# Optimization experiments

Hardware: AMD Instinct MI355X
Metric: run time of the kernel (lower is better)

## Reference

```python
import jax, jax.numpy as jnp
import numpy as np

BN_EPS = 1e-5
STRIDE = 12          # ACCENT_DOWNSAMPLE_STRIDE
NQ = 8               # ACCENT_VQ_QUANTIZERS
K = 256              # ACCENT_VQ_CODEBOOK_SIZE
VQ_D = 16            # ACCENT_VQ_DIM
EMB = 128            # ACCENT_EMBEDDING_DIM


def conv1d(x, w, b, stride=1, padding=0):
    # x: (B, Cin, T), w: (Cout, Cin, Kw)
    y = jax.lax.conv_general_dilated(
        x, w, window_strides=(stride,), padding=[(padding, padding)],
        dimension_numbers=("NCW", "OIW", "NCW"))
    return y + b[None, :, None]


def batchnorm(x, gamma, beta, mean, var):
    # eval-mode BatchNorm1d over channel dim
    inv = jax.lax.rsqrt(var + BN_EPS)
    return (x - mean[None, :, None]) * (inv * gamma)[None, :, None] + beta[None, :, None]


def setup_inputs() -> dict:
    key = jax.random.key(0)
    ks = jax.random.split(key, 12)
    C = 256
    d = {
        "mel_spectrogram": jax.random.normal(ks[0], (16, 80, 4096), jnp.float32),
        "w1": jax.random.normal(ks[1], (C, 80, 5), jnp.float32) * 0.05,
        "b1": jnp.zeros((C,), jnp.float32),
        "g1": jnp.ones((C,), jnp.float32),
        "be1": jnp.zeros((C,), jnp.float32),
        "m1": jax.random.normal(ks[2], (C,), jnp.float32) * 0.1,
        "v1": jax.random.uniform(ks[3], (C,), jnp.float32, 0.5, 1.5),
        "w2": jax.random.normal(ks[4], (C, C, 5), jnp.float32) * 0.03,
        "b2": jnp.zeros((C,), jnp.float32),
        "g2": jnp.ones((C,), jnp.float32),
        "be2": jnp.zeros((C,), jnp.float32),
        "m2": jax.random.normal(ks[5], (C,), jnp.float32) * 0.1,
        "v2": jax.random.uniform(ks[6], (C,), jnp.float32, 0.5, 1.5),
        "wd": jax.random.normal(ks[7], (EMB, C, 2 * STRIDE), jnp.float32) * 0.02,
        "bd": jnp.zeros((EMB,), jnp.float32),
        "wp": jax.random.normal(ks[8], (VQ_D, EMB, 1), jnp.float32) * 0.1,
        "bp": jnp.zeros((VQ_D,), jnp.float32),
        "codebooks": jax.random.normal(ks[9], (NQ, K, VQ_D), jnp.float32) * 0.3,
    }
    return d


def reference(mel_spectrogram, w1, b1, g1, be1, m1, v1,
              w2, b2, g2, be2, m2, v2, wd, bd, wp, bp, codebooks):
    # CNN stack
    x = jax.nn.relu(batchnorm(conv1d(mel_spectrogram, w1, b1, 1, 2), g1, be1, m1, v1))
    x = jax.nn.relu(batchnorm(conv1d(x, w2, b2, 1, 2), g2, be2, m2, v2))
    # Downsample conv: kernel=24, stride=12, pad=6
    e_a_unq = conv1d(x, wd, bd, STRIDE, STRIDE // 2)          # (B, 128, T')
    z = conv1d(e_a_unq, wp, bp, 1, 0)                          # (B, 16, T')
    # RVQ: 8 sequential cdist-argmin-subtract steps
    r = jnp.transpose(z, (0, 2, 1))                            # (B, T', 16)
    idx_list = []
    for q in range(NQ):
        cb = codebooks[q]                                      # (K, 16)
        # squared euclidean distances (B, T', K)
        d = (jnp.sum(r * r, -1, keepdims=True)
             - 2.0 * jnp.einsum("btd,kd->btk", r, cb)
             + jnp.sum(cb * cb, -1))
        idx = jnp.argmin(d, axis=-1)                           # (B, T')
        idx_list.append(idx)
        r = r - cb[idx]                                        # residual update
    indices = jnp.stack(idx_list, axis=0)                      # (NQ, B, T')
    return e_a_unq, indices
```

## Files before the change

kernel.cpp:

```cpp
#include <hip/hip_runtime.h>
#include <math.h>

#define B_    16
#define T_    4096
#define C_    256
#define CIN1  80
#define EMB   128
#define TP    341
#define NPOS  (B_*TP)
#define NQ_   8
#define KCB   256
#define BN_EPS 1e-5

__global__ __launch_bounds__(256) void prep_v7(
    const float* __restrict__ w2, const float* __restrict__ wd,
    const float* __restrict__ b1, const float* __restrict__ g1,
    const float* __restrict__ be1, const float* __restrict__ m1,
    const float* __restrict__ v1,
    const float* __restrict__ b2, const float* __restrict__ g2,
    const float* __restrict__ be2, const float* __restrict__ m2,
    const float* __restrict__ v2,
    float* __restrict__ w2t, float* __restrict__ wdt,
    double* __restrict__ a1, double* __restrict__ bt1,
    double* __restrict__ a2, double* __restrict__ bt2)
{
    int j = blockIdx.x * 256 + threadIdx.x;
    if (j < 256*24*128) wdt[j] = wd[(size_t)(j & 127) * 6144 + (j >> 7)];
    if (j < 256*5*256)  w2t[j] = w2[(size_t)(j & 255) * 1280 + (j >> 8)];
    if (j < 256) {
        double inv1 = 1.0 / sqrt((double)v1[j] + BN_EPS);
        double s1 = (double)g1[j] * inv1;
        a1[j]  = s1;
        bt1[j] = ((double)b1[j] - (double)m1[j]) * s1 + (double)be1[j];
        double inv2 = 1.0 / sqrt((double)v2[j] + BN_EPS);
        double s2 = (double)g2[j] * inv2;
        a2[j]  = s2;
        bt2[j] = ((double)b2[j] - (double)m2[j]) * s2 + (double)be2[j];
    }
}

__device__ __forceinline__ int swz_pair(int col) {
    int bw = col >> 1;
    return ((bw ^ ((bw >> 3) & 7)) << 1);
}
__device__ __forceinline__ int swz_scalar(int col) {
    int bw = col >> 1;
    return (((bw ^ ((bw >> 3) & 7)) << 1) | (col & 1));
}

template<int CIN, typename Tin, bool TR>
__global__ __launch_bounds__(256) void conv5_bn_relu_f64(
    const Tin* __restrict__ in,
    const float* __restrict__ wt,
    const double* __restrict__ alpha, const double* __restrict__ beta,
    double* __restrict__ out)
{
    const int b   = blockIdx.z;
    const int co0 = blockIdx.y * 64;
    const int t0  = blockIdx.x * 128;
    const int tid = threadIdx.x;
    const int tcol = tid & 15;
    const int trow = tid >> 4;

    __shared__ double xs[8][136];
    __shared__ double wsh[40][64];

    double acc[4][8];
    #pragma unroll
    for (int i = 0; i < 4; ++i)
        #pragma unroll
        for (int j = 0; j < 8; ++j) acc[i][j] = 0.0;

    for (int c0 = 0; c0 < CIN; c0 += 8) {
        for (int i = tid; i < 8 * 132; i += 256) {
            int ci = i / 132, col = i % 132;
            int t = t0 - 2 + col;
            double v = 0.0;
            if (t >= 0 && t < T_) v = (double)in[((size_t)(b * CIN + c0 + ci)) * T_ + t];
            xs[ci][swz_scalar(col)] = v;
        }
        for (int i = tid; i < 40 * 64; i += 256) {
            int r = i >> 6, co = i & 63;
            float wv;
            if (TR) wv = wt[(size_t)(c0 * 5 + r) * 256 + co0 + co];
            else    wv = wt[(size_t)(co0 + co) * (CIN * 5) + c0 * 5 + r];
            wsh[r][co] = (double)wv;
        }
        __syncthreads();

        #pragma unroll
        for (int ci = 0; ci < 8; ++ci) {
            double xv[12];
            #pragma unroll
            for (int m = 0; m < 6; ++m) {
                double2 v = *(const double2*)&xs[ci][swz_pair(tcol * 8 + 2 * m)];
                xv[2 * m] = v.x; xv[2 * m + 1] = v.y;
            }
            #pragma unroll
            for (int k = 0; k < 5; ++k) {
                double w0 = wsh[ci * 5 + k][trow * 4 + 0];
                double w1v = wsh[ci * 5 + k][trow * 4 + 1];
                double w2v = wsh[ci * 5 + k][trow * 4 + 2];
                double w3v = wsh[ci * 5 + k][trow * 4 + 3];
                #pragma unroll
                for (int j = 0; j < 8; ++j) {
                    double xq = xv[j + k];
                    acc[0][j] = fma(w0, xq, acc[0][j]);
                    acc[1][j] = fma(w1v, xq, acc[1][j]);
                    acc[2][j] = fma(w2v, xq, acc[2][j]);
                    acc[3][j] = fma(w3v, xq, acc[3][j]);
                }
            }
        }
        __syncthreads();
    }

    const int cobase = co0 + trow * 4;
    const int tg = t0 + tcol * 8;
    #pragma unroll
    for (int i = 0; i < 4; ++i) {
        double a = alpha[cobase + i], bt = beta[cobase + i];
        size_t base = ((size_t)(b * C_ + cobase + i)) * T_ + tg;
        #pragma unroll
        for (int j = 0; j < 8; ++j) {
            double y = fma(acc[i][j], a, bt);
            out[base + j] = y > 0.0 ? y : 0.0;
        }
    }
}

__global__ __launch_bounds__(256) void convd_f64_v6(
    const double* __restrict__ x2,
    const float* __restrict__ wdt,
    double* __restrict__ parts,
    int nb, int nsplit, int cis)
{
    const int bz  = blockIdx.z;
    const int s   = bz % nsplit;
    const int b   = bz / nsplit;
    const int tp0 = blockIdx.x * 64;
    const int tid = threadIdx.x;
    const int tcol = tid & 15;
    const int crow = tid >> 4;

    __shared__ double xs2[2][24][66];
    __shared__ double wsh[48][128];

    double acc[8][4];
    #pragma unroll
    for (int i = 0; i < 8; ++i)
        #pragma unroll
        for (int j = 0; j < 4; ++j) acc[i][j] = 0.0;

    const int tbase = tp0 * 12 - 6;
    const int ci_begin = s * cis;

    for (int c0 = ci_begin; c0 < ci_begin + cis; c0 += 2) {
        for (int i = tid; i < 2 * 780; i += 256) {
            int ci = (i >= 780) ? 1 : 0;
            int c = i - ci * 780;
            int t = tbase + c;
            double v = (t >= 0 && t < T_)
                ? x2[((size_t)(b * 256 + c0 + ci)) * T_ + t] : 0.0;
            int tp = (c * 43691) >> 19;
            int kp = c - tp * 12;
            xs2[ci][kp][tp] = v;
            if (tp >= 1) xs2[ci][kp + 12][tp - 1] = v;
        }
        for (int i = tid; i < 48 * 128; i += 256) {
            int r = i >> 7, c = i & 127;
            wsh[r][c] = (double)wdt[(size_t)(c0 * 24 + r) * 128 + c];
        }
        __syncthreads();

        const double* xb = &xs2[0][0][0] + tcol;
        const double* wb = &wsh[0][0] + crow * 8;
        #pragma unroll
        for (int ci = 0; ci < 2; ++ci) {
            #pragma unroll
            for (int k = 0; k < 24; ++k) {
                double wv[8], xv[4];
                #pragma unroll
                for (int i = 0; i < 8; ++i) wv[i] = wb[(ci * 24 + k) * 128 + i];
                #pragma unroll
                for (int j = 0; j < 4; ++j) xv[j] = xb[(ci * 24 + k) * 66 + 16 * j];
                #pragma unroll
                for (int i = 0; i < 8; ++i)
                    #pragma unroll
                    for (int j = 0; j < 4; ++j)
                        acc[i][j] = fma(wv[i], xv[j], acc[i][j]);
            }
        }
        __syncthreads();
    }

    #pragma unroll
    for (int i = 0; i < 8; ++i) {
        int co = crow * 8 + i;
        #pragma unroll
        for (int j = 0; j < 4; ++j) {
            int tp = tp0 + tcol + 16 * j;
            if (tp < TP)
                parts[(((size_t)s * nb + b) * EMB + co) * TP + tp] = acc[i][j];
        }
    }
}

__global__ __launch_bounds__(256) void convd_combine(
    double* __restrict__ parts,
    const float* __restrict__ bd,
    float* __restrict__ e_out,
    int nb, int b_off, int nsplit)
{
    int idx = blockIdx.x * 256 + threadIdx.x;
    int total = nb * EMB * TP;
    if (idx >= total) return;
    int rem = idx % (EMB * TP);
    int co = rem / TP;
    int b_local = idx / (EMB * TP);
    size_t stride = (size_t)nb * EMB * TP;
    double y = 0.0;
    for (int s = 0; s < nsplit; ++s)
        y += parts[(size_t)s * stride + idx];
    y += (double)bd[co];
    parts[idx] = y;
    e_out[(size_t)b_off * EMB * TP + idx] = (float)y;
}

__global__ __launch_bounds__(128) void zproj_f64(
    const double* __restrict__ ed,
    const float* __restrict__ wp,
    const float* __restrict__ bp,
    double* __restrict__ z)
{
    const int b = blockIdx.y;
    const int t = blockIdx.x * 128 + threadIdx.x;
    __shared__ double wps[16][128];
    for (int i = threadIdx.x; i < 16 * 128; i += 128)
        wps[i >> 7][i & 127] = (double)wp[i];
    __syncthreads();
    if (t >= TP) return;
    double acc[16];
    #pragma unroll
    for (int v = 0; v < 16; ++v) acc[v] = (double)bp[v];
    for (int co = 0; co < 128; ++co) {
        double x = ed[((size_t)(b * EMB + co)) * TP + t];
        #pragma unroll
        for (int v = 0; v < 16; ++v) acc[v] = fma(x, wps[v][co], acc[v]);
    }
    #pragma unroll
    for (int v = 0; v < 16; ++v)
        z[((size_t)(b * TP + t)) * 16 + v] = acc[v];
}

__global__ __launch_bounds__(256) void rvq_f64_v2(
    const double* __restrict__ z,
    const float* __restrict__ cb,
    float* __restrict__ out_idx)
{
    const int pos = blockIdx.x;
    const int tid = threadIdx.x;
    const int lane = tid & 63;
    const int wv = tid >> 6;

    __shared__ double r[16];
    __shared__ double wd_s[4];
    __shared__ int wi_s[4];
    __shared__ int best_s;

    if (tid < 16) r[tid] = z[(size_t)pos * 16 + tid];
    __syncthreads();

    for (int q = 0; q < NQ_; ++q) {
        const float* c = cb + ((size_t)(q * KCB) + tid) * 16;
        double d = 0.0;
        #pragma unroll
        for (int i = 0; i < 16; ++i) {
            double diff = r[i] - (double)c[i];
            d = fma(diff, diff, d);
        }
        int idx = tid;
        #pragma unroll
        for (int sft = 32; sft > 0; sft >>= 1) {
            double d2 = __shfl_down(d, sft, 64);
            int i2 = __shfl_down(idx, sft, 64);
            if (d2 < d || (d2 == d && i2 < idx)) { d = d2; idx = i2; }
        }
        if (lane == 0) { wd_s[wv] = d; wi_s[wv] = idx; }
        __syncthreads();
        if (tid == 0) {
            double bd_ = wd_s[0]; int bi = wi_s[0];
            #pragma unroll
            for (int w = 1; w < 4; ++w) {
                if (wd_s[w] < bd_ || (wd_s[w] == bd_ && wi_s[w] < bi)) {
                    bd_ = wd_s[w]; bi = wi_s[w];
                }
            }
            best_s = bi;
            out_idx[(size_t)q * NPOS + pos] = (float)bi;
        }
        __syncthreads();
        int best = best_s;
        if (tid < 16)
            r[tid] = r[tid] - (double)cb[((size_t)(q * KCB) + best) * 16 + tid];
        __syncthreads();
    }
}

extern "C" void kernel_launch(void* const* d_in, const int* in_sizes, int n_in,
                              void* d_out, int out_size, void* d_ws, size_t ws_size,
                              hipStream_t stream) {
    const float* mel = (const float*)d_in[0];
    const float* w1  = (const float*)d_in[1];
    const float* b1  = (const float*)d_in[2];
    const float* g1  = (const float*)d_in[3];
    const float* be1 = (const float*)d_in[4];
    const float* m1  = (const float*)d_in[5];
    const float* v1  = (const float*)d_in[6];
    const float* w2  = (const float*)d_in[7];
    const float* b2  = (const float*)d_in[8];
    const float* g2  = (const float*)d_in[9];
    const float* be2 = (const float*)d_in[10];
    const float* m2  = (const float*)d_in[11];
    const float* v2  = (const float*)d_in[12];
    const float* wd  = (const float*)d_in[13];
    const float* bd  = (const float*)d_in[14];
    const float* wp  = (const float*)d_in[15];
    const float* bp  = (const float*)d_in[16];
    const float* cb  = (const float*)d_in[17];

    const int nb = 8;
    const int ngrp = B_ / nb;
    const int nsplit = 16;
    const int cis = 256 / nsplit;

    auto al = [](size_t x) { return (x + 255) & ~(size_t)255; };
    const size_t x1_big   = (size_t)nb * C_ * T_ * 8;
    const size_t x1_small = (size_t)4  * C_ * T_ * 8;
    const size_t parts_b  = (size_t)nsplit * nb * EMB * TP * 8;
    const size_t x2_bytes = (size_t)nb * C_ * T_ * 8;
    const size_t tail = al((size_t)256*5*256*4)
                      + al((size_t)256*24*128*4)
                      + 4 * al(2048)
                      + al((size_t)B_ * TP * 16 * 8);
    const size_t need_big = al(x1_big) + al(x2_bytes) + tail;

    const bool big = (ws_size >= need_big);
    const int cc = big ? 8 : 4;
    const size_t shared_bytes = big ? x1_big
                                    : (x1_small > parts_b ? x1_small : parts_b);

    char* ws = (char*)d_ws;
    size_t off = 0;
    auto alloc = [&](size_t bytes) -> char* {
        char* p = ws + off;
        off = (off + bytes + 255) & ~(size_t)255;
        return p;
    };
    char* shared = alloc(shared_bytes);
    double* x1d  = (double*)shared;
    double* parts= (double*)shared;
    double* x2d  = (double*)alloc(x2_bytes);
    float*  w2t  = (float*)alloc((size_t)256*5*256*4);
    float*  wdt  = (float*)alloc((size_t)256*24*128*4);
    double* a1d  = (double*)alloc(2048);
    double* bt1d = (double*)alloc(2048);
    double* a2d  = (double*)alloc(2048);
    double* bt2d = (double*)alloc(2048);
    double* zd   = (double*)alloc((size_t)B_ * TP * 16 * 8);

    float* e_out   = (float*)d_out;
    float* idx_out = (float*)d_out + (size_t)B_ * EMB * TP;

    prep_v7<<<3072, 256, 0, stream>>>(w2, wd, b1, g1, be1, m1, v1,
                                      b2, g2, be2, m2, v2,
                                      w2t, wdt, a1d, bt1d, a2d, bt2d);

    const int comb_blocks = (nb * EMB * TP + 255) / 256;
    for (int g = 0; g < ngrp; ++g) {
        for (int ch = 0; ch < nb / cc; ++ch) {
            int b_abs = g * nb + ch * cc;
            conv5_bn_relu_f64<CIN1, float, false>
                <<<dim3(32, 4, cc), 256, 0, stream>>>(
                mel + (size_t)b_abs * CIN1 * T_, w1, a1d, bt1d,
                x1d + (big ? (size_t)ch * cc * C_ * T_ : 0));
            conv5_bn_relu_f64<C_, double, true>
                <<<dim3(32, 4, cc), 256, 0, stream>>>(
                x1d + (big ? (size_t)ch * cc * C_ * T_ : 0), w2t, a2d, bt2d,
                x2d + (size_t)ch * cc * C_ * T_);
        }
        convd_f64_v6<<<dim3(6, 1, nb * nsplit), 256, 0, stream>>>(
            x2d, wdt, parts, nb, nsplit, cis);
        convd_combine<<<comb_blocks, 256, 0, stream>>>(
            parts, bd, e_out, nb, g * nb, nsplit);
        zproj_f64<<<dim3(3, nb), 128, 0, stream>>>(
            parts, wp, bp, zd + (size_t)g * nb * TP * 16);
    }
    rvq_f64_v2<<<NPOS, 256, 0, stream>>>(zd, cb, idx_out);
}
```

Baseline: 1.902 ms.

## Enlarge register tiles in fp64 conv and downsample kernels for more reuse

The conv5 kernels now compute 256 time steps per block with 4x16 accumulators per thread, and weights are loaded into registers with vectorised double2 reads. The downsample conv processes 128 output positions per block, one input channel per iteration, with 8x8 accumulators per thread and swizzled shared memory. The aim is to raise the FMA-to-shared-load ratio in these fp64 loops and halve the block count. In exchange, register pressure goes up, the launch bounds now request two blocks per SM, and there are fewer blocks to fill the GPU.

Result: faster. 1.781 ms (-6.4%).

```diff
diff --git a/kernel.cpp b/kernel.cpp
--- a/kernel.cpp
+++ b/kernel.cpp
@@ -49,7 +49,7 @@
 }
 
 template<int CIN, typename Tin, bool TR>
-__global__ __launch_bounds__(256) void conv5_bn_relu_f64(
+__global__ __launch_bounds__(256, 2) void conv5_v8(
     const Tin* __restrict__ in,
     const float* __restrict__ wt,
     const double* __restrict__ alpha, const double* __restrict__ beta,
@@ -57,23 +57,23 @@
 {
     const int b   = blockIdx.z;
     const int co0 = blockIdx.y * 64;
-    const int t0  = blockIdx.x * 128;
+    const int t0  = blockIdx.x * 256;
     const int tid = threadIdx.x;
     const int tcol = tid & 15;
     const int trow = tid >> 4;
 
-    __shared__ double xs[8][136];
-    __shared__ double wsh[40][64];
-
-    double acc[4][8];
+    __shared__ __align__(16) double xs[8][264];
+    __shared__ __align__(16) double wsh[40][64];
+
+    double acc[4][16];
     #pragma unroll
     for (int i = 0; i < 4; ++i)
         #pragma unroll
-        for (int j = 0; j < 8; ++j) acc[i][j] = 0.0;
+        for (int j = 0; j < 16; ++j) acc[i][j] = 0.0;
 
     for (int c0 = 0; c0 < CIN; c0 += 8) {
-        for (int i = tid; i < 8 * 132; i += 256) {
-            int ci = i / 132, col = i % 132;
+        for (int i = tid; i < 8 * 260; i += 256) {
+            int ci = i / 260, col = i - ci * 260;
             int t = t0 - 2 + col;
             double v = 0.0;
             if (t >= 0 && t < T_) v = (double)in[((size_t)(b * CIN + c0 + ci)) * T_ + t];
@@ -88,48 +88,57 @@
         }
         __syncthreads();
 
-        #pragma unroll
+        #pragma unroll 2
         for (int ci = 0; ci < 8; ++ci) {
-            double xv[12];
-            #pragma unroll
-            for (int m = 0; m < 6; ++m) {
-                double2 v = *(const double2*)&xs[ci][swz_pair(tcol * 8 + 2 * m)];
-                xv[2 * m] = v.x; xv[2 * m + 1] = v.y;
-            }
+            double wv[20];
             #pragma unroll
             for (int k = 0; k < 5; ++k) {
-                double w0 = wsh[ci * 5 + k][trow * 4 + 0];
-                double w1v = wsh[ci * 5 + k][trow * 4 + 1];
-                double w2v = wsh[ci * 5 + k][trow * 4 + 2];
-                double w3v = wsh[ci * 5 + k][trow * 4 + 3];
+                double2 wa = *(const double2*)&wsh[ci * 5 + k][trow * 4];
+                double2 wb = *(const double2*)&wsh[ci * 5 + k][trow * 4 + 2];
+                wv[k * 4 + 0] = wa.x; wv[k * 4 + 1] = wa.y;
+                wv[k * 4 + 2] = wb.x; wv[k * 4 + 3] = wb.y;
+            }
+            #pragma unroll
+            for (int h = 0; h < 2; ++h) {
+                double xv[12];
                 #pragma unroll
-                for (int j = 0; j < 8; ++j) {
-                    double xq = xv[j + k];
-                    acc[0][j] = fma(w0, xq, acc[0][j]);
-                    acc[1][j] = fma(w1v, xq, acc[1][j]);
-                    acc[2][j] = fma(w2v, xq, acc[2][j]);
-                    acc[3][j] = fma(w3v, xq, acc[3][j]);
+                for (int m = 0; m < 6; ++m) {
+                    double2 v2 = *(const double2*)&xs[ci][swz_pair(tcol * 16 + h * 8 + 2 * m)];
+                    xv[2 * m] = v2.x; xv[2 * m + 1] = v2.y;
                 }
+                #pragma unroll
+                for (int k = 0; k < 5; ++k)
+                    #pragma unroll
+                    for (int i4 = 0; i4 < 4; ++i4) {
+                        double w = wv[k * 4 + i4];
+                        #pragma unroll
+                        for (int j = 0; j < 8; ++j)
+                            acc[i4][h * 8 + j] = fma(w, xv[j + k], acc[i4][h * 8 + j]);
+                    }
             }
         }
         __syncthreads();
     }
 
     const int cobase = co0 + trow * 4;
-    const int tg = t0 + tcol * 8;
-    #pragma unroll
-    for (int i = 0; i < 4; ++i) {
-        double a = alpha[cobase + i], bt = beta[cobase + i];
-        size_t base = ((size_t)(b * C_ + cobase + i)) * T_ + tg;
-        #pragma unroll
-        for (int j = 0; j < 8; ++j) {
-            double y = fma(acc[i][j], a, bt);
-            out[base + j] = y > 0.0 ? y : 0.0;
-        }
-    }
-}
-
-__global__ __launch_bounds__(256) void convd_f64_v6(
+    const int tg = t0 + tcol * 16;
+    #pragma unroll
+    for (int i4 = 0; i4 < 4; ++i4) {
+        double a = alpha[cobase + i4], bt = beta[cobase + i4];
+        size_t base = ((size_t)(b * C_ + cobase + i4)) * T_ + tg;
+        #pragma unroll
+        for (int m = 0; m < 8; ++m) {
+            double2 o;
+            double y0 = fma(acc[i4][2 * m], a, bt);
+            double y1 = fma(acc[i4][2 * m + 1], a, bt);
+            o.x = y0 > 0.0 ? y0 : 0.0;
+            o.y = y1 > 0.0 ? y1 : 0.0;
+            *(double2*)&out[base + 2 * m] = o;
+        }
+    }
+}
+
+__global__ __launch_bounds__(256, 2) void convd_f64_v7(
     const double* __restrict__ x2,
     const float* __restrict__ wdt,
     double* __restrict__ parts,
@@ -138,57 +147,55 @@
     const int bz  = blockIdx.z;
     const int s   = bz % nsplit;
     const int b   = bz / nsplit;
-    const int tp0 = blockIdx.x * 64;
+    const int tp0 = blockIdx.x * 128;
     const int tid = threadIdx.x;
     const int tcol = tid & 15;
     const int crow = tid >> 4;
 
-    __shared__ double xs2[2][24][66];
-    __shared__ double wsh[48][128];
-
-    double acc[8][4];
+    __shared__ __align__(16) double xs2[24][132];
+    __shared__ __align__(16) double wsh[24][128];
+
+    double acc[8][8];
     #pragma unroll
     for (int i = 0; i < 8; ++i)
         #pragma unroll
-        for (int j = 0; j < 4; ++j) acc[i][j] = 0.0;
+        for (int j = 0; j < 8; ++j) acc[i][j] = 0.0;
 
     const int tbase = tp0 * 12 - 6;
     const int ci_begin = s * cis;
 
-    for (int c0 = ci_begin; c0 < ci_begin + cis; c0 += 2) {
-        for (int i = tid; i < 2 * 780; i += 256) {
-            int ci = (i >= 780) ? 1 : 0;
-            int c = i - ci * 780;
-            int t = tbase + c;
+    for (int c = ci_begin; c < ci_begin + cis; ++c) {
+        for (int i = tid; i < 1548; i += 256) {
+            int t = tbase + i;
             double v = (t >= 0 && t < T_)
-                ? x2[((size_t)(b * 256 + c0 + ci)) * T_ + t] : 0.0;
-            int tp = (c * 43691) >> 19;
-            int kp = c - tp * 12;
-            xs2[ci][kp][tp] = v;
-            if (tp >= 1) xs2[ci][kp + 12][tp - 1] = v;
-        }
-        for (int i = tid; i < 48 * 128; i += 256) {
-            int r = i >> 7, c = i & 127;
-            wsh[r][c] = (double)wdt[(size_t)(c0 * 24 + r) * 128 + c];
-        }
-        __syncthreads();
-
-        const double* xb = &xs2[0][0][0] + tcol;
-        const double* wb = &wsh[0][0] + crow * 8;
-        #pragma unroll
-        for (int ci = 0; ci < 2; ++ci) {
-            #pragma unroll
-            for (int k = 0; k < 24; ++k) {
-                double wv[8], xv[4];
+                ? x2[((size_t)(b * 256 + c)) * T_ + t] : 0.0;
+            int tp = (i * 43691) >> 19;
+            int kp = i - tp * 12;
+            xs2[kp][swz_scalar(tp)] = v;
+            if (tp >= 1) xs2[kp + 12][swz_scalar(tp - 1)] = v;
+        }
+        for (int i = tid; i < 24 * 128; i += 256) {
+            int r = i >> 7, cc = i & 127;
+            wsh[r][cc] = (double)wdt[((size_t)c * 24 + r) * 128 + cc];
+        }
+        __syncthreads();
+
+        #pragma unroll 4
+        for (int k = 0; k < 24; ++k) {
+            double wv[8];
+            #pragma unroll
+            for (int m = 0; m < 4; ++m) {
+                double2 w2v = *(const double2*)&wsh[k][crow * 8 + 2 * m];
+                wv[2 * m] = w2v.x; wv[2 * m + 1] = w2v.y;
+            }
+            #pragma unroll
+            for (int jp = 0; jp < 4; ++jp) {
+                double2 xp = *(const double2*)&xs2[k][swz_pair(tcol * 2 + 32 * jp)];
                 #pragma unroll
-                for (int i = 0; i < 8; ++i) wv[i] = wb[(ci * 24 + k) * 128 + i];
-                #pragma unroll
-                for (int j = 0; j < 4; ++j) xv[j] = xb[(ci * 24 + k) * 66 + 16 * j];
-                #pragma unroll
-                for (int i = 0; i < 8; ++i)
-                    #pragma unroll
-                    for (int j = 0; j < 4; ++j)
-                        acc[i][j] = fma(wv[i], xv[j], acc[i][j]);
+                for (int i = 0; i < 8; ++i) {
+                    acc[i][jp * 2]     = fma(wv[i], xp.x, acc[i][jp * 2]);
+                    acc[i][jp * 2 + 1] = fma(wv[i], xp.y, acc[i][jp * 2 + 1]);
+                }
             }
         }
         __syncthreads();
@@ -198,10 +205,13 @@
     for (int i = 0; i < 8; ++i) {
         int co = crow * 8 + i;
         #pragma unroll
-        for (int j = 0; j < 4; ++j) {
-            int tp = tp0 + tcol + 16 * j;
-            if (tp < TP)
-                parts[(((size_t)s * nb + b) * EMB + co) * TP + tp] = acc[i][j];
+        for (int jp = 0; jp < 4; ++jp) {
+            #pragma unroll
+            for (int e = 0; e < 2; ++e) {
+                int tp = tp0 + tcol * 2 + 32 * jp + e;
+                if (tp < TP)
+                    parts[(((size_t)s * nb + b) * EMB + co) * TP + tp] = acc[i][jp * 2 + e];
+            }
         }
     }
 }
@@ -217,7 +227,6 @@
     if (idx >= total) return;
     int rem = idx % (EMB * TP);
     int co = rem / TP;
-    int b_local = idx / (EMB * TP);
     size_t stride = (size_t)nb * EMB * TP;
     double y = 0.0;
     for (int s = 0; s < nsplit; ++s)
@@ -380,16 +389,16 @@
     for (int g = 0; g < ngrp; ++g) {
         for (int ch = 0; ch < nb / cc; ++ch) {
             int b_abs = g * nb + ch * cc;
-            conv5_bn_relu_f64<CIN1, float, false>
-                <<<dim3(32, 4, cc), 256, 0, stream>>>(
+            conv5_v8<CIN1, float, false>
+                <<<dim3(16, 4, cc), 256, 0, stream>>>(
                 mel + (size_t)b_abs * CIN1 * T_, w1, a1d, bt1d,
                 x1d + (big ? (size_t)ch * cc * C_ * T_ : 0));
-            conv5_bn_relu_f64<C_, double, true>
-                <<<dim3(32, 4, cc), 256, 0, stream>>>(
+            conv5_v8<C_, double, true>
+                <<<dim3(16, 4, cc), 256, 0, stream>>>(
                 x1d + (big ? (size_t)ch * cc * C_ * T_ : 0), w2t, a2d, bt2d,
                 x2d + (size_t)ch * cc * C_ * T_);
         }
-        convd_f64_v6<<<dim3(6, 1, nb * nsplit), 256, 0, stream>>>(
+        convd_f64_v7<<<dim3(3, 1, nb * nsplit), 256, 0, stream>>>(
             x2d, wdt, parts, nb, nsplit, cis);
         convd_combine<<<comb_blocks, 256, 0, stream>>>(
             parts, bd, e_out, nb, g * nb, nsplit);
```
